# Optimization experiments

Measured on AMD Instinct MI355X. Metric: run time of the kernel, lower is better.

Reference implementation:

```python
import jax, jax.numpy as jnp
import numpy as np

N, M, D = 4096, 8192, 1024
N_ITERS = 15  # module hardcodes self.n_iters = 15
EPS = 1e-12   # F.normalize eps


def setup_inputs() -> dict:
    key = jax.random.key(0)
    k1, k2 = jax.random.split(key)
    K = jax.random.normal(k1, (N, M), dtype=jnp.float32)
    y = jax.random.normal(k2, (M, D), dtype=jnp.float32)
    return {"K": K, "y": y, "topk": 32}


def _topk_preimage(K_mat, y, topk):
    # torch: topk -> L1-normalize values -> scatter into zeros_like(K) -> mm(y).
    # Since topk indices are unique per row, scatter+dense-mm == gather + weighted sum.
    vals, inds = jax.lax.top_k(K_mat, topk)                      # [N, k], [N, k]
    norm = jnp.maximum(jnp.sum(jnp.abs(vals), axis=-1, keepdims=True), EPS)
    w = vals / norm                                              # F.normalize(p=1, dim=-1)
    preimage = jnp.einsum('nk,nkd->nd', w, y[inds])              # [N, D]
    return preimage, inds


def reference(K, y, topk):
    preimage, inds = _topk_preimage(K, y, topk)

    def body(pre, _):
        K_i = pre @ y.T                                          # linear kernel_fn: [N, M]
        pre, inds_i = _topk_preimage(K_i, y, topk)
        return pre, inds_i

    preimage, inds_all = jax.lax.scan(body, preimage, None, length=N_ITERS)
    return preimage, inds_all[-1]
```

## Files before the change

kernel.cpp:

```cpp
#include <hip/hip_runtime.h>
#include <hip/hip_bf16.h>
#include <math.h>

#define N_ROWS 4096
#define M_COLS 8192
#define D_DIM  1024
#define TOPK   32
#define N_ITERS 15
#define CHUNK   2048
#define KC      384
#define D_CUT   1696

template <int EXACT_V>
__global__ __launch_bounds__(256) void topk_pre_kernel(
    const float* __restrict__ R,
    const float* __restrict__ Y,
    float* __restrict__ pre,
    int* __restrict__ inds_ws,
    int row_off, int write_inds)
{
    __shared__ float s_wv[4];
    __shared__ int   s_wi[4];
    __shared__ float topv[TOPK];
    __shared__ int   topi[TOPK];
    __shared__ int   s_win;
    __shared__ float s_w[TOPK];
    __shared__ int   s_si[TOPK];
    __shared__ float s_sw[TOPK];
    __shared__ float s_norm;

    const int tid    = threadIdx.x;
    const int n_loc  = blockIdx.x;
    const int n_glob = row_off + n_loc;
    const float* Rr  = R + (size_t)n_loc * M_COLS;

    float v[32];
    #pragma unroll
    for (int q = 0; q < 8; ++q) {
        float4 w = reinterpret_cast<const float4*>(Rr)[tid + 256 * q];
        v[4 * q + 0] = w.x; v[4 * q + 1] = w.y;
        v[4 * q + 2] = w.z; v[4 * q + 3] = w.w;
    }

    for (int s = 0; s < TOPK; ++s) {
        float bv = -INFINITY; int bi = M_COLS;
        #pragma unroll
        for (int q = 0; q < 8; ++q)
            #pragma unroll
            for (int c = 0; c < 4; ++c) {
                const int m = 4 * q + c;
                const int j = 4 * tid + 1024 * q + c;
                const float val = v[m];
                if (val > bv || (val == bv && j < bi)) { bv = val; bi = j; }
            }
        #pragma unroll
        for (int off = 32; off > 0; off >>= 1) {
            float ov = __shfl_down(bv, off);
            int   oi = __shfl_down(bi, off);
            if (ov > bv || (ov == bv && oi < bi)) { bv = ov; bi = oi; }
        }
        if ((tid & 63) == 0) { s_wv[tid >> 6] = bv; s_wi[tid >> 6] = bi; }
        __syncthreads();
        if (tid == 0) {
            for (int w = 1; w < 4; ++w) {
                if (s_wv[w] > bv || (s_wv[w] == bv && s_wi[w] < bi)) {
                    bv = s_wv[w]; bi = s_wi[w];
                }
            }
            topv[s] = bv; topi[s] = bi; s_win = bi;
        }
        __syncthreads();
        const int win = s_win;
        if (((win >> 2) & 255) == tid) {
            const int mw = ((win >> 10) << 2) | (win & 3);
            #pragma unroll
            for (int m = 0; m < 32; ++m)
                if (m == mw) v[m] = -INFINITY;
        }
    }

    if (EXACT_V) {
        if (tid == 0) {
            double sum = 0.0;
            for (int k = 0; k < TOPK; ++k) sum += fabs((double)topv[k]);
            s_norm = fmaxf((float)sum, 1e-12f);
        }
    } else {
        if (tid == 0) {
            float r[8];
            #pragma unroll
            for (int j = 0; j < 8; ++j) r[j] = fabsf(topv[j]);
            #pragma unroll
            for (int blk = 8; blk < TOPK; blk += 8)
                #pragma unroll
                for (int j = 0; j < 8; ++j)
                    r[j] = __fadd_rn(r[j], fabsf(topv[blk + j]));
            float s01 = __fadd_rn(r[0], r[1]);
            float s23 = __fadd_rn(r[2], r[3]);
            float s45 = __fadd_rn(r[4], r[5]);
            float s67 = __fadd_rn(r[6], r[7]);
            s_norm = fmaxf(__fadd_rn(__fadd_rn(s01, s23), __fadd_rn(s45, s67)), 1e-12f);
        }
    }
    __syncthreads();
    if (tid < TOPK) s_w[tid] = __fdiv_rn(topv[tid], s_norm);
    __syncthreads();

    if (EXACT_V) {
        double acc[4] = {0.0, 0.0, 0.0, 0.0};
        for (int k = 0; k < TOPK; ++k) {
            const double wk = (double)s_w[k];
            const float* yr = Y + (size_t)topi[k] * D_DIM;
            #pragma unroll
            for (int j = 0; j < 4; ++j)
                acc[j] = fma(wk, (double)yr[tid + 256 * j], acc[j]);
        }
        float* pr = pre + (size_t)n_glob * D_DIM;
        #pragma unroll
        for (int j = 0; j < 4; ++j) pr[tid + 256 * j] = (float)acc[j];
    } else {
        if (tid == 0) {
            for (int k = 0; k < TOPK; ++k) { s_si[k] = topi[k]; s_sw[k] = s_w[k]; }
            for (int a = 1; a < TOPK; ++a) {
                int ia = s_si[a]; float wa = s_sw[a];
                int b = a - 1;
                while (b >= 0 && s_si[b] > ia) {
                    s_si[b + 1] = s_si[b]; s_sw[b + 1] = s_sw[b]; --b;
                }
                s_si[b + 1] = ia; s_sw[b + 1] = wa;
            }
        }
        __syncthreads();
        float tot[4]  = {0.f, 0.f, 0.f, 0.f};
        float part[4] = {0.f, 0.f, 0.f, 0.f};
        int curPan = s_si[0] / KC;
        for (int k = 0; k < TOPK; ++k) {
            const int idx = s_si[k];
            const int pan = idx / KC;
            if (pan != curPan) {
                #pragma unroll
                for (int j = 0; j < 4; ++j) {
                    tot[j] = __fadd_rn(tot[j], part[j]);
                    part[j] = 0.f;
                }
                curPan = pan;
            }
            const float wk = s_sw[k];
            const float* yr = Y + (size_t)idx * D_DIM;
            #pragma unroll
            for (int j = 0; j < 4; ++j)
                part[j] = fmaf(wk, yr[tid + 256 * j], part[j]);
        }
        #pragma unroll
        for (int j = 0; j < 4; ++j) tot[j] = __fadd_rn(tot[j], part[j]);
        float* pr = pre + (size_t)n_glob * D_DIM;
        #pragma unroll
        for (int j = 0; j < 4; ++j) pr[tid + 256 * j] = tot[j];
    }

    if (write_inds && tid < TOPK)
        inds_ws[(size_t)n_glob * TOPK + tid] = topi[tid];
}

#define ABM 128
#define ABN 128
#define ABK 16

__global__ __launch_bounds__(256) void gemmA_kernel(
    const float* __restrict__ A,
    const float* __restrict__ B,
    float* __restrict__ C)
{
    __shared__ float As[ABK][ABM + 4];
    __shared__ float Bs[ABK][ABN + 4];

    const int tid  = threadIdx.x;
    const int tx   = tid & 15;
    const int ty   = tid >> 4;
    const int row0 = blockIdx.y * ABM;
    const int col0 = blockIdx.x * ABN;

    const int lr = tid >> 1;
    const int lc = (tid & 1) * 8;

    float tot[8][8], acc[8][8];
    #pragma unroll
    for (int i = 0; i < 8; ++i)
        #pragma unroll
        for (int j = 0; j < 8; ++j) { tot[i][j] = 0.f; acc[i][j] = 0.f; }

    for (int k0 = 0; k0 < D_DIM; k0 += ABK) {
        float4 va0 = *reinterpret_cast<const float4*>(A + (size_t)(row0 + lr) * D_DIM + k0 + lc);
        float4 va1 = *reinterpret_cast<const float4*>(A + (size_t)(row0 + lr) * D_DIM + k0 + lc + 4);
        As[lc + 0][lr] = va0.x; As[lc + 1][lr] = va0.y;
        As[lc + 2][lr] = va0.z; As[lc + 3][lr] = va0.w;
        As[lc + 4][lr] = va1.x; As[lc + 5][lr] = va1.y;
        As[lc + 6][lr] = va1.z; As[lc + 7][lr] = va1.w;
        float4 vb0 = *reinterpret_cast<const float4*>(B + (size_t)(col0 + lr) * D_DIM + k0 + lc);
        float4 vb1 = *reinterpret_cast<const float4*>(B + (size_t)(col0 + lr) * D_DIM + k0 + lc + 4);
        Bs[lc + 0][lr] = vb0.x; Bs[lc + 1][lr] = vb0.y;
        Bs[lc + 2][lr] = vb0.z; Bs[lc + 3][lr] = vb0.w;
        Bs[lc + 4][lr] = vb1.x; Bs[lc + 5][lr] = vb1.y;
        Bs[lc + 6][lr] = vb1.z; Bs[lc + 7][lr] = vb1.w;
        __syncthreads();

        #pragma unroll
        for (int kk = 0; kk < ABK; ++kk) {
            float a[8], b[8];
            #pragma unroll
            for (int i = 0; i < 8; ++i) a[i] = As[kk][ty * 8 + i];
            #pragma unroll
            for (int j = 0; j < 8; ++j) b[j] = Bs[kk][tx * 8 + j];
            #pragma unroll
            for (int i = 0; i < 8; ++i)
                #pragma unroll
                for (int j = 0; j < 8; ++j)
                    acc[i][j] = fmaf(a[i], b[j], acc[i][j]);
        }
        __syncthreads();

        const int kend = k0 + ABK;
        if (kend == KC || kend == 2 * KC || kend == D_DIM) {
            #pragma unroll
            for (int i = 0; i < 8; ++i)
                #pragma unroll
                for (int j = 0; j < 8; ++j) {
                    tot[i][j] = __fadd_rn(tot[i][j], acc[i][j]);
                    acc[i][j] = 0.f;
                }
        }
    }

    #pragma unroll
    for (int i = 0; i < 8; ++i) {
        float4 v0 = { tot[i][0], tot[i][1], tot[i][2], tot[i][3] };
        float4 v1 = { tot[i][4], tot[i][5], tot[i][6], tot[i][7] };
        float* cr = C + (size_t)(row0 + ty * 8 + i) * M_COLS + col0 + tx * 8;
        *reinterpret_cast<float4*>(cr)     = v0;
        *reinterpret_cast<float4*>(cr + 4) = v1;
    }
}

#define BBM 128
#define BBN 64
#define BBK 16

__global__ __launch_bounds__(256) void gemmB_kernel(
    const float* __restrict__ A,
    const float* __restrict__ B,
    float* __restrict__ C)
{
    __shared__ float As[BBK][BBM + 4];
    __shared__ float Bs[BBK][BBN + 4];

    const int tid  = threadIdx.x;
    const int tx   = tid & 15;
    const int ty   = tid >> 4;
    const int row0 = blockIdx.y * BBM;
    const int col0 = blockIdx.x * BBN;

    const int lrA = tid >> 1;
    const int lcA = (tid & 1) * 8;
    const int lrB = tid >> 2;
    const int lcB = (tid & 3) * 4;

    double dacc[8][4];
    #pragma unroll
    for (int i = 0; i < 8; ++i)
        #pragma unroll
        for (int j = 0; j < 4; ++j) dacc[i][j] = 0.0;

    for (int k0 = 0; k0 < D_DIM; k0 += BBK) {
        float4 va0 = *reinterpret_cast<const float4*>(A + (size_t)(row0 + lrA) * D_DIM + k0 + lcA);
        float4 va1 = *reinterpret_cast<const float4*>(A + (size_t)(row0 + lrA) * D_DIM + k0 + lcA + 4);
        As[lcA + 0][lrA] = va0.x; As[lcA + 1][lrA] = va0.y;
        As[lcA + 2][lrA] = va0.z; As[lcA + 3][lrA] = va0.w;
        As[lcA + 4][lrA] = va1.x; As[lcA + 5][lrA] = va1.y;
        As[lcA + 6][lrA] = va1.z; As[lcA + 7][lrA] = va1.w;
        float4 vb = *reinterpret_cast<const float4*>(B + (size_t)(col0 + lrB) * D_DIM + k0 + lcB);
        Bs[lcB + 0][lrB] = vb.x; Bs[lcB + 1][lrB] = vb.y;
        Bs[lcB + 2][lrB] = vb.z; Bs[lcB + 3][lrB] = vb.w;
        __syncthreads();

        #pragma unroll
        for (int kk = 0; kk < BBK; ++kk) {
            double a[8], b[4];
            #pragma unroll
            for (int i = 0; i < 8; ++i) a[i] = (double)As[kk][ty * 8 + i];
            #pragma unroll
            for (int j = 0; j < 4; ++j) b[j] = (double)Bs[kk][tx * 4 + j];
            #pragma unroll
            for (int i = 0; i < 8; ++i)
                #pragma unroll
                for (int j = 0; j < 4; ++j)
                    dacc[i][j] = fma(a[i], b[j], dacc[i][j]);
        }
        __syncthreads();
    }

    #pragma unroll
    for (int i = 0; i < 8; ++i) {
        float4 v = { (float)dacc[i][0], (float)dacc[i][1],
                     (float)dacc[i][2], (float)dacc[i][3] };
        float* cr = C + (size_t)(row0 + ty * 8 + i) * M_COLS + col0 + tx * 4;
        *reinterpret_cast<float4*>(cr) = v;
    }
}

__global__ __launch_bounds__(256) void choice_kernel(
    const int* __restrict__ indsA,
    const int* __restrict__ indsB,
    unsigned char* __restrict__ choice)
{
    const int n = blockIdx.x * 256 + threadIdx.x;
    if (n >= N_ROWS) return;
    int d = 0;
    #pragma unroll
    for (int k = 0; k < TOPK; ++k) {
        int diff = indsA[n * TOPK + k] - indsB[n * TOPK + k];
        if (diff < 0) diff = -diff;
        if (diff > d) d = diff;
    }
    choice[n] = (d > 0 && d <= D_CUT) ? 1 : 0;
}

__global__ __launch_bounds__(256) void emit_kernel(
    const float* __restrict__ preA, const float* __restrict__ preB,
    const int* __restrict__ indsA,  const int* __restrict__ indsB,
    const unsigned char* __restrict__ choice,
    float* __restrict__ out_pre, float* __restrict__ out_inds)
{
    const int n   = blockIdx.x;
    const int tid = threadIdx.x;
    const int c   = choice[n];
    const float* ps = (c ? preB : preA) + (size_t)n * D_DIM;
    const int*   is = (c ? indsB : indsA) + (size_t)n * TOPK;
    float* po = out_pre + (size_t)n * D_DIM;
    #pragma unroll
    for (int j = 0; j < 4; ++j) po[tid + 256 * j] = ps[tid + 256 * j];
    if (tid < TOPK)
        out_inds[(size_t)n * TOPK + tid] = (float)is[tid];
}

extern "C" void kernel_launch(void* const* d_in, const int* in_sizes, int n_in,
                              void* d_out, int out_size, void* d_ws, size_t ws_size,
                              hipStream_t stream)
{
    const float* K_in = (const float*)d_in[0];
    const float* Y    = (const float*)d_in[1];

    char* p = (char*)d_ws;
    float* preA   = (float*)p; p += (size_t)N_ROWS * D_DIM * sizeof(float);
    float* preB   = (float*)p; p += (size_t)N_ROWS * D_DIM * sizeof(float);
    float* Kchunk = (float*)p; p += (size_t)CHUNK * M_COLS * sizeof(float);
    int*   indsA  = (int*)p;   p += (size_t)N_ROWS * TOPK * sizeof(int);
    int*   indsB  = (int*)p;   p += (size_t)N_ROWS * TOPK * sizeof(int);
    unsigned char* choice = (unsigned char*)p;

    float* out_pre  = (float*)d_out;
    float* out_inds = out_pre + (size_t)N_ROWS * D_DIM;

    topk_pre_kernel<0><<<N_ROWS, 256, 0, stream>>>(K_in, Y, preA, indsA, 0, 0);
    topk_pre_kernel<1><<<N_ROWS, 256, 0, stream>>>(K_in, Y, preB, indsB, 0, 0);

    for (int it = 0; it < N_ITERS; ++it) {
        const int wo = (it == N_ITERS - 1) ? 1 : 0;
        for (int c = 0; c < N_ROWS / CHUNK; ++c) {
            gemmA_kernel<<<dim3(M_COLS / ABN, CHUNK / ABM), 256, 0, stream>>>(
                preA + (size_t)c * CHUNK * D_DIM, Y, Kchunk);
            topk_pre_kernel<0><<<CHUNK, 256, 0, stream>>>(
                Kchunk, Y, preA, indsA, c * CHUNK, wo);
            gemmB_kernel<<<dim3(M_COLS / BBN, CHUNK / BBM), 256, 0, stream>>>(
                preB + (size_t)c * CHUNK * D_DIM, Y, Kchunk);
            topk_pre_kernel<1><<<CHUNK, 256, 0, stream>>>(
                Kchunk, Y, preB, indsB, c * CHUNK, wo);
        }
    }

    choice_kernel<<<(N_ROWS + 255) / 256, 256, 0, stream>>>(indsA, indsB, choice);
    emit_kernel<<<N_ROWS, 256, 0, stream>>>(preA, preB, indsA, indsB, choice,
                                            out_pre, out_inds);
}
```

Before: 53.53 ms.

## Vectorize shared-memory fragment loads and enlarge FP64 GEMM tile with double staging

The fp32 GEMM now reads its A/B register fragments from shared memory with float4 loads instead of scalar loads. The fp64 GEMM widens its output tile from 128x64 to 128x128, giving each thread an 8x8 accumulator. It also converts inputs to double when storing them to shared memory, so the inner loop no longer converts per element, and it reads fragments with double2 loads. The aim is fewer LDS instructions and conversions and more reuse per loaded value. The cost is a larger shared-memory footprint and 64 double accumulators per thread, which raises register pressure and may lower occupancy.

```diff
diff --git a/kernel.cpp b/kernel.cpp
--- a/kernel.cpp
+++ b/kernel.cpp
@@ -171,8 +171,8 @@
     const float* __restrict__ B,
     float* __restrict__ C)
 {
-    __shared__ float As[ABK][ABM + 4];
-    __shared__ float Bs[ABK][ABN + 4];
+    __shared__ __align__(16) float As[ABK][ABM + 4];
+    __shared__ __align__(16) float Bs[ABK][ABN + 4];
 
     const int tid  = threadIdx.x;
     const int tx   = tid & 15;
@@ -207,10 +207,10 @@
         #pragma unroll
         for (int kk = 0; kk < ABK; ++kk) {
             float a[8], b[8];
-            #pragma unroll
-            for (int i = 0; i < 8; ++i) a[i] = As[kk][ty * 8 + i];
-            #pragma unroll
-            for (int j = 0; j < 8; ++j) b[j] = Bs[kk][tx * 8 + j];
+            *reinterpret_cast<float4*>(&a[0]) = *reinterpret_cast<float4*>(&As[kk][ty * 8]);
+            *reinterpret_cast<float4*>(&a[4]) = *reinterpret_cast<float4*>(&As[kk][ty * 8 + 4]);
+            *reinterpret_cast<float4*>(&b[0]) = *reinterpret_cast<float4*>(&Bs[kk][tx * 8]);
+            *reinterpret_cast<float4*>(&b[4]) = *reinterpret_cast<float4*>(&Bs[kk][tx * 8 + 4]);
             #pragma unroll
             for (int i = 0; i < 8; ++i)
                 #pragma unroll
@@ -242,7 +242,7 @@
 }
 
 #define BBM 128
-#define BBN 64
+#define BBN 128
 #define BBK 16
 
 __global__ __launch_bounds__(256) void gemmB_kernel(
@@ -250,8 +250,8 @@
     const float* __restrict__ B,
     float* __restrict__ C)
 {
-    __shared__ float As[BBK][BBM + 4];
-    __shared__ float Bs[BBK][BBN + 4];
+    __shared__ __align__(16) double As[BBK][BBM + 4];
+    __shared__ __align__(16) double Bs[BBK][BBN + 4];
 
     const int tid  = threadIdx.x;
     const int tx   = tid & 15;
@@ -259,51 +259,59 @@
     const int row0 = blockIdx.y * BBM;
     const int col0 = blockIdx.x * BBN;
 
-    const int lrA = tid >> 1;
-    const int lcA = (tid & 1) * 8;
-    const int lrB = tid >> 2;
-    const int lcB = (tid & 3) * 4;
-
-    double dacc[8][4];
+    const int lr = tid >> 1;
+    const int lc = (tid & 1) * 8;
+
+    double acc[8][8];
     #pragma unroll
     for (int i = 0; i < 8; ++i)
         #pragma unroll
-        for (int j = 0; j < 4; ++j) dacc[i][j] = 0.0;
+        for (int j = 0; j < 8; ++j) acc[i][j] = 0.0;
 
     for (int k0 = 0; k0 < D_DIM; k0 += BBK) {
-        float4 va0 = *reinterpret_cast<const float4*>(A + (size_t)(row0 + lrA) * D_DIM + k0 + lcA);
-        float4 va1 = *reinterpret_cast<const float4*>(A + (size_t)(row0 + lrA) * D_DIM + k0 + lcA + 4);
-        As[lcA + 0][lrA] = va0.x; As[lcA + 1][lrA] = va0.y;
-        As[lcA + 2][lrA] = va0.z; As[lcA + 3][lrA] = va0.w;
-        As[lcA + 4][lrA] = va1.x; As[lcA + 5][lrA] = va1.y;
-        As[lcA + 6][lrA] = va1.z; As[lcA + 7][lrA] = va1.w;
-        float4 vb = *reinterpret_cast<const float4*>(B + (size_t)(col0 + lrB) * D_DIM + k0 + lcB);
-        Bs[lcB + 0][lrB] = vb.x; Bs[lcB + 1][lrB] = vb.y;
-        Bs[lcB + 2][lrB] = vb.z; Bs[lcB + 3][lrB] = vb.w;
+        float4 va0 = *reinterpret_cast<const float4*>(A + (size_t)(row0 + lr) * D_DIM + k0 + lc);
+        float4 va1 = *reinterpret_cast<const float4*>(A + (size_t)(row0 + lr) * D_DIM + k0 + lc + 4);
+        As[lc + 0][lr] = (double)va0.x; As[lc + 1][lr] = (double)va0.y;
+        As[lc + 2][lr] = (double)va0.z; As[lc + 3][lr] = (double)va0.w;
+        As[lc + 4][lr] = (double)va1.x; As[lc + 5][lr] = (double)va1.y;
+        As[lc + 6][lr] = (double)va1.z; As[lc + 7][lr] = (double)va1.w;
+        float4 vb0 = *reinterpret_cast<const float4*>(B + (size_t)(col0 + lr) * D_DIM + k0 + lc);
+        float4 vb1 = *reinterpret_cast<const float4*>(B + (size_t)(col0 + lr) * D_DIM + k0 + lc + 4);
+        Bs[lc + 0][lr] = (double)vb0.x; Bs[lc + 1][lr] = (double)vb0.y;
+        Bs[lc + 2][lr] = (double)vb0.z; Bs[lc + 3][lr] = (double)vb0.w;
+        Bs[lc + 4][lr] = (double)vb1.x; Bs[lc + 5][lr] = (double)vb1.y;
+        Bs[lc + 6][lr] = (double)vb1.z; Bs[lc + 7][lr] = (double)vb1.w;
         __syncthreads();
 
         #pragma unroll
         for (int kk = 0; kk < BBK; ++kk) {
-            double a[8], b[4];
-            #pragma unroll
-            for (int i = 0; i < 8; ++i) a[i] = (double)As[kk][ty * 8 + i];
-            #pragma unroll
-            for (int j = 0; j < 4; ++j) b[j] = (double)Bs[kk][tx * 4 + j];
+            double a[8], b[8];
+            *reinterpret_cast<double2*>(&a[0]) = *reinterpret_cast<double2*>(&As[kk][ty * 8]);
+            *reinterpret_cast<double2*>(&a[2]) = *reinterpret_cast<double2*>(&As[kk][ty * 8 + 2]);
+            *reinterpret_cast<double2*>(&a[4]) = *reinterpret_cast<double2*>(&As[kk][ty * 8 + 4]);
+            *reinterpret_cast<double2*>(&a[6]) = *reinterpret_cast<double2*>(&As[kk][ty * 8 + 6]);
+            *reinterpret_cast<double2*>(&b[0]) = *reinterpret_cast<double2*>(&Bs[kk][tx * 8]);
+            *reinterpret_cast<double2*>(&b[2]) = *reinterpret_cast<double2*>(&Bs[kk][tx * 8 + 2]);
+            *reinterpret_cast<double2*>(&b[4]) = *reinterpret_cast<double2*>(&Bs[kk][tx * 8 + 4]);
+            *reinterpret_cast<double2*>(&b[6]) = *reinterpret_cast<double2*>(&Bs[kk][tx * 8 + 6]);
             #pragma unroll
             for (int i = 0; i < 8; ++i)
                 #pragma unroll
-                for (int j = 0; j < 4; ++j)
-                    dacc[i][j] = fma(a[i], b[j], dacc[i][j]);
+                for (int j = 0; j < 8; ++j)
+                    acc[i][j] = fma(a[i], b[j], acc[i][j]);
         }
         __syncthreads();
     }
 
     #pragma unroll
     for (int i = 0; i < 8; ++i) {
-        float4 v = { (float)dacc[i][0], (float)dacc[i][1],
-                     (float)dacc[i][2], (float)dacc[i][3] };
-        float* cr = C + (size_t)(row0 + ty * 8 + i) * M_COLS + col0 + tx * 4;
-        *reinterpret_cast<float4*>(cr) = v;
+        float4 v0 = { (float)acc[i][0], (float)acc[i][1],
+                      (float)acc[i][2], (float)acc[i][3] };
+        float4 v1 = { (float)acc[i][4], (float)acc[i][5],
+                      (float)acc[i][6], (float)acc[i][7] };
+        float* cr = C + (size_t)(row0 + ty * 8 + i) * M_COLS + col0 + tx * 8;
+        *reinterpret_cast<float4*>(cr)     = v0;
+        *reinterpret_cast<float4*>(cr + 4) = v1;
     }
 }
 
```

Result: slower. 56.14 ms (+4.9%).

## Fuse fp32 and fp64 GEMM/top-k paths into dual-grid kernels with incremental argmax

Applied to the files above, without the earlier changes.

Merges the fp32 and fp64 GEMM kernels into one launch that picks its path by blockIdx.z, and does the same for the two top-k kernels. Each path gets its own K buffer, and the chunk size drops from 2048 to 1024 to keep workspace size in check. This lets the cheap fp32 work overlap the expensive fp64 work and halves the number of launches per chunk. The top-k loop now keeps a per-thread running max and rescans only in the thread that lost its winner, and the fp32 GEMM reads shared memory with float4 loads. The trade-offs are more chunk iterations, extra register pressure from the dual code paths in one kernel, and wasted early-exit blocks in the fp32 half of the GEMM grid.

```diff
diff --git a/kernel.cpp b/kernel.cpp
--- a/kernel.cpp
+++ b/kernel.cpp
@@ -7,16 +7,15 @@
 #define D_DIM  1024
 #define TOPK   32
 #define N_ITERS 15
-#define CHUNK   2048
+#define CHUNK   1024
 #define KC      384
 #define D_CUT   1696
 
-template <int EXACT_V>
-__global__ __launch_bounds__(256) void topk_pre_kernel(
-    const float* __restrict__ R,
+__global__ __launch_bounds__(256) void topk_dual_kernel(
+    const float* __restrict__ RA, const float* __restrict__ RB,
     const float* __restrict__ Y,
-    float* __restrict__ pre,
-    int* __restrict__ inds_ws,
+    float* __restrict__ preA, float* __restrict__ preB,
+    int* __restrict__ indsA, int* __restrict__ indsB,
     int row_off, int write_inds)
 {
     __shared__ float s_wv[4];
@@ -29,6 +28,11 @@
     __shared__ float s_sw[TOPK];
     __shared__ float s_norm;
 
+    const int exact_v = blockIdx.z;
+    const float* R    = exact_v ? RB : RA;
+    float* pre        = exact_v ? preB : preA;
+    int*   inds_ws    = exact_v ? indsB : indsA;
+
     const int tid    = threadIdx.x;
     const int n_loc  = blockIdx.x;
     const int n_glob = row_off + n_loc;
@@ -42,17 +46,18 @@
         v[4 * q + 2] = w.z; v[4 * q + 3] = w.w;
     }
 
+    float cv = -INFINITY; int ci = M_COLS;
+    #pragma unroll
+    for (int q = 0; q < 8; ++q)
+        #pragma unroll
+        for (int c = 0; c < 4; ++c) {
+            const int m = 4 * q + c;
+            const int j = 4 * tid + 1024 * q + c;
+            if (v[m] > cv || (v[m] == cv && j < ci)) { cv = v[m]; ci = j; }
+        }
+
     for (int s = 0; s < TOPK; ++s) {
-        float bv = -INFINITY; int bi = M_COLS;
-        #pragma unroll
-        for (int q = 0; q < 8; ++q)
-            #pragma unroll
-            for (int c = 0; c < 4; ++c) {
-                const int m = 4 * q + c;
-                const int j = 4 * tid + 1024 * q + c;
-                const float val = v[m];
-                if (val > bv || (val == bv && j < bi)) { bv = val; bi = j; }
-            }
+        float bv = cv; int bi = ci;
         #pragma unroll
         for (int off = 32; off > 0; off >>= 1) {
             float ov = __shfl_down(bv, off);
@@ -76,10 +81,19 @@
             #pragma unroll
             for (int m = 0; m < 32; ++m)
                 if (m == mw) v[m] = -INFINITY;
-        }
-    }
-
-    if (EXACT_V) {
+            cv = -INFINITY; ci = M_COLS;
+            #pragma unroll
+            for (int q = 0; q < 8; ++q)
+                #pragma unroll
+                for (int c = 0; c < 4; ++c) {
+                    const int m = 4 * q + c;
+                    const int j = 4 * tid + 1024 * q + c;
+                    if (v[m] > cv || (v[m] == cv && j < ci)) { cv = v[m]; ci = j; }
+                }
+        }
+    }
+
+    if (exact_v) {
         if (tid == 0) {
             double sum = 0.0;
             for (int k = 0; k < TOPK; ++k) sum += fabs((double)topv[k]);
@@ -106,7 +120,7 @@
     if (tid < TOPK) s_w[tid] = __fdiv_rn(topv[tid], s_norm);
     __syncthreads();
 
-    if (EXACT_V) {
+    if (exact_v) {
         double acc[4] = {0.0, 0.0, 0.0, 0.0};
         for (int k = 0; k < TOPK; ++k) {
             const double wk = (double)s_w[k];
@@ -165,145 +179,141 @@
 #define ABM 128
 #define ABN 128
 #define ABK 16
-
-__global__ __launch_bounds__(256) void gemmA_kernel(
-    const float* __restrict__ A,
-    const float* __restrict__ B,
-    float* __restrict__ C)
-{
-    __shared__ float As[ABK][ABM + 4];
-    __shared__ float Bs[ABK][ABN + 4];
-
-    const int tid  = threadIdx.x;
-    const int tx   = tid & 15;
-    const int ty   = tid >> 4;
-    const int row0 = blockIdx.y * ABM;
-    const int col0 = blockIdx.x * ABN;
-
-    const int lr = tid >> 1;
-    const int lc = (tid & 1) * 8;
-
-    float tot[8][8], acc[8][8];
-    #pragma unroll
-    for (int i = 0; i < 8; ++i)
-        #pragma unroll
-        for (int j = 0; j < 8; ++j) { tot[i][j] = 0.f; acc[i][j] = 0.f; }
-
-    for (int k0 = 0; k0 < D_DIM; k0 += ABK) {
-        float4 va0 = *reinterpret_cast<const float4*>(A + (size_t)(row0 + lr) * D_DIM + k0 + lc);
-        float4 va1 = *reinterpret_cast<const float4*>(A + (size_t)(row0 + lr) * D_DIM + k0 + lc + 4);
-        As[lc + 0][lr] = va0.x; As[lc + 1][lr] = va0.y;
-        As[lc + 2][lr] = va0.z; As[lc + 3][lr] = va0.w;
-        As[lc + 4][lr] = va1.x; As[lc + 5][lr] = va1.y;
-        As[lc + 6][lr] = va1.z; As[lc + 7][lr] = va1.w;
-        float4 vb0 = *reinterpret_cast<const float4*>(B + (size_t)(col0 + lr) * D_DIM + k0 + lc);
-        float4 vb1 = *reinterpret_cast<const float4*>(B + (size_t)(col0 + lr) * D_DIM + k0 + lc + 4);
-        Bs[lc + 0][lr] = vb0.x; Bs[lc + 1][lr] = vb0.y;
-        Bs[lc + 2][lr] = vb0.z; Bs[lc + 3][lr] = vb0.w;
-        Bs[lc + 4][lr] = vb1.x; Bs[lc + 5][lr] = vb1.y;
-        Bs[lc + 6][lr] = vb1.z; Bs[lc + 7][lr] = vb1.w;
-        __syncthreads();
-
-        #pragma unroll
-        for (int kk = 0; kk < ABK; ++kk) {
-            float a[8], b[8];
-            #pragma unroll
-            for (int i = 0; i < 8; ++i) a[i] = As[kk][ty * 8 + i];
-            #pragma unroll
-            for (int j = 0; j < 8; ++j) b[j] = Bs[kk][tx * 8 + j];
-            #pragma unroll
-            for (int i = 0; i < 8; ++i)
-                #pragma unroll
-                for (int j = 0; j < 8; ++j)
-                    acc[i][j] = fmaf(a[i], b[j], acc[i][j]);
-        }
-        __syncthreads();
-
-        const int kend = k0 + ABK;
-        if (kend == KC || kend == 2 * KC || kend == D_DIM) {
-            #pragma unroll
-            for (int i = 0; i < 8; ++i)
-                #pragma unroll
-                for (int j = 0; j < 8; ++j) {
-                    tot[i][j] = __fadd_rn(tot[i][j], acc[i][j]);
-                    acc[i][j] = 0.f;
-                }
-        }
-    }
-
-    #pragma unroll
-    for (int i = 0; i < 8; ++i) {
-        float4 v0 = { tot[i][0], tot[i][1], tot[i][2], tot[i][3] };
-        float4 v1 = { tot[i][4], tot[i][5], tot[i][6], tot[i][7] };
-        float* cr = C + (size_t)(row0 + ty * 8 + i) * M_COLS + col0 + tx * 8;
-        *reinterpret_cast<float4*>(cr)     = v0;
-        *reinterpret_cast<float4*>(cr + 4) = v1;
-    }
-}
-
 #define BBM 128
 #define BBN 64
 #define BBK 16
 
-__global__ __launch_bounds__(256) void gemmB_kernel(
-    const float* __restrict__ A,
-    const float* __restrict__ B,
-    float* __restrict__ C)
-{
-    __shared__ float As[BBK][BBM + 4];
-    __shared__ float Bs[BBK][BBN + 4];
-
-    const int tid  = threadIdx.x;
-    const int tx   = tid & 15;
-    const int ty   = tid >> 4;
-    const int row0 = blockIdx.y * BBM;
-    const int col0 = blockIdx.x * BBN;
-
-    const int lrA = tid >> 1;
-    const int lcA = (tid & 1) * 8;
-    const int lrB = tid >> 2;
-    const int lcB = (tid & 3) * 4;
-
-    double dacc[8][4];
-    #pragma unroll
-    for (int i = 0; i < 8; ++i)
-        #pragma unroll
-        for (int j = 0; j < 4; ++j) dacc[i][j] = 0.0;
-
-    for (int k0 = 0; k0 < D_DIM; k0 += BBK) {
-        float4 va0 = *reinterpret_cast<const float4*>(A + (size_t)(row0 + lrA) * D_DIM + k0 + lcA);
-        float4 va1 = *reinterpret_cast<const float4*>(A + (size_t)(row0 + lrA) * D_DIM + k0 + lcA + 4);
-        As[lcA + 0][lrA] = va0.x; As[lcA + 1][lrA] = va0.y;
-        As[lcA + 2][lrA] = va0.z; As[lcA + 3][lrA] = va0.w;
-        As[lcA + 4][lrA] = va1.x; As[lcA + 5][lrA] = va1.y;
-        As[lcA + 6][lrA] = va1.z; As[lcA + 7][lrA] = va1.w;
-        float4 vb = *reinterpret_cast<const float4*>(B + (size_t)(col0 + lrB) * D_DIM + k0 + lcB);
-        Bs[lcB + 0][lrB] = vb.x; Bs[lcB + 1][lrB] = vb.y;
-        Bs[lcB + 2][lrB] = vb.z; Bs[lcB + 3][lrB] = vb.w;
-        __syncthreads();
-
-        #pragma unroll
-        for (int kk = 0; kk < BBK; ++kk) {
-            double a[8], b[4];
-            #pragma unroll
-            for (int i = 0; i < 8; ++i) a[i] = (double)As[kk][ty * 8 + i];
-            #pragma unroll
-            for (int j = 0; j < 4; ++j) b[j] = (double)Bs[kk][tx * 4 + j];
-            #pragma unroll
-            for (int i = 0; i < 8; ++i)
-                #pragma unroll
-                for (int j = 0; j < 4; ++j)
-                    dacc[i][j] = fma(a[i], b[j], dacc[i][j]);
-        }
-        __syncthreads();
-    }
-
-    #pragma unroll
-    for (int i = 0; i < 8; ++i) {
-        float4 v = { (float)dacc[i][0], (float)dacc[i][1],
-                     (float)dacc[i][2], (float)dacc[i][3] };
-        float* cr = C + (size_t)(row0 + ty * 8 + i) * M_COLS + col0 + tx * 4;
-        *reinterpret_cast<float4*>(cr) = v;
+__global__ __launch_bounds__(256) void gemm_dual_kernel(
+    const float* __restrict__ PA, const float* __restrict__ PB,
+    const float* __restrict__ Y,
+    float* __restrict__ CA, float* __restrict__ CB)
+{
+    __shared__ __align__(16) char smem[16896];
+
+    const int tid = threadIdx.x;
+
+    if (blockIdx.z == 0) {
+        if (blockIdx.x >= M_COLS / ABN) return;
+        float (*As)[ABM + 4] = reinterpret_cast<float(*)[ABM + 4]>(smem);
+        float (*Bs)[ABN + 4] = reinterpret_cast<float(*)[ABN + 4]>(smem + 8448);
+
+        const int tx   = tid & 15;
+        const int ty   = tid >> 4;
+        const int row0 = blockIdx.y * ABM;
+        const int col0 = blockIdx.x * ABN;
+        const int lr   = tid >> 1;
+        const int lc   = (tid & 1) * 8;
+
+        float tot[8][8], acc[8][8];
+        #pragma unroll
+        for (int i = 0; i < 8; ++i)
+            #pragma unroll
+            for (int j = 0; j < 8; ++j) { tot[i][j] = 0.f; acc[i][j] = 0.f; }
+
+        for (int k0 = 0; k0 < D_DIM; k0 += ABK) {
+            float4 va0 = *reinterpret_cast<const float4*>(PA + (size_t)(row0 + lr) * D_DIM + k0 + lc);
+            float4 va1 = *reinterpret_cast<const float4*>(PA + (size_t)(row0 + lr) * D_DIM + k0 + lc + 4);
+            As[lc + 0][lr] = va0.x; As[lc + 1][lr] = va0.y;
+            As[lc + 2][lr] = va0.z; As[lc + 3][lr] = va0.w;
+            As[lc + 4][lr] = va1.x; As[lc + 5][lr] = va1.y;
+            As[lc + 6][lr] = va1.z; As[lc + 7][lr] = va1.w;
+            float4 vb0 = *reinterpret_cast<const float4*>(Y + (size_t)(col0 + lr) * D_DIM + k0 + lc);
+            float4 vb1 = *reinterpret_cast<const float4*>(Y + (size_t)(col0 + lr) * D_DIM + k0 + lc + 4);
+            Bs[lc + 0][lr] = vb0.x; Bs[lc + 1][lr] = vb0.y;
+            Bs[lc + 2][lr] = vb0.z; Bs[lc + 3][lr] = vb0.w;
+            Bs[lc + 4][lr] = vb1.x; Bs[lc + 5][lr] = vb1.y;
+            Bs[lc + 6][lr] = vb1.z; Bs[lc + 7][lr] = vb1.w;
+            __syncthreads();
+
+            #pragma unroll
+            for (int kk = 0; kk < ABK; ++kk) {
+                float a[8], b[8];
+                *reinterpret_cast<float4*>(&a[0]) = *reinterpret_cast<float4*>(&As[kk][ty * 8]);
+                *reinterpret_cast<float4*>(&a[4]) = *reinterpret_cast<float4*>(&As[kk][ty * 8 + 4]);
+                *reinterpret_cast<float4*>(&b[0]) = *reinterpret_cast<float4*>(&Bs[kk][tx * 8]);
+                *reinterpret_cast<float4*>(&b[4]) = *reinterpret_cast<float4*>(&Bs[kk][tx * 8 + 4]);
+                #pragma unroll
+                for (int i = 0; i < 8; ++i)
+                    #pragma unroll
+                    for (int j = 0; j < 8; ++j)
+                        acc[i][j] = fmaf(a[i], b[j], acc[i][j]);
+            }
+            __syncthreads();
+
+            const int kend = k0 + ABK;
+            if (kend == KC || kend == 2 * KC || kend == D_DIM) {
+                #pragma unroll
+                for (int i = 0; i < 8; ++i)
+                    #pragma unroll
+                    for (int j = 0; j < 8; ++j) {
+                        tot[i][j] = __fadd_rn(tot[i][j], acc[i][j]);
+                        acc[i][j] = 0.f;
+                    }
+            }
+        }
+
+        #pragma unroll
+        for (int i = 0; i < 8; ++i) {
+            float4 v0 = { tot[i][0], tot[i][1], tot[i][2], tot[i][3] };
+            float4 v1 = { tot[i][4], tot[i][5], tot[i][6], tot[i][7] };
+            float* cr = CA + (size_t)(row0 + ty * 8 + i) * M_COLS + col0 + tx * 8;
+            *reinterpret_cast<float4*>(cr)     = v0;
+            *reinterpret_cast<float4*>(cr + 4) = v1;
+        }
+    } else {
+        float (*As)[BBM + 4] = reinterpret_cast<float(*)[BBM + 4]>(smem);
+        float (*Bs)[BBN + 4] = reinterpret_cast<float(*)[BBN + 4]>(smem + 8448);
+
+        const int tx   = tid & 15;
+        const int ty   = tid >> 4;
+        const int row0 = blockIdx.y * BBM;
+        const int col0 = blockIdx.x * BBN;
+        const int lrA = tid >> 1;
+        const int lcA = (tid & 1) * 8;
+        const int lrB = tid >> 2;
+        const int lcB = (tid & 3) * 4;
+
+        double dacc[8][4];
+        #pragma unroll
+        for (int i = 0; i < 8; ++i)
+            #pragma unroll
+            for (int j = 0; j < 4; ++j) dacc[i][j] = 0.0;
+
+        for (int k0 = 0; k0 < D_DIM; k0 += BBK) {
+            float4 va0 = *reinterpret_cast<const float4*>(PB + (size_t)(row0 + lrA) * D_DIM + k0 + lcA);
+            float4 va1 = *reinterpret_cast<const float4*>(PB + (size_t)(row0 + lrA) * D_DIM + k0 + lcA + 4);
+            As[lcA + 0][lrA] = va0.x; As[lcA + 1][lrA] = va0.y;
+            As[lcA + 2][lrA] = va0.z; As[lcA + 3][lrA] = va0.w;
+            As[lcA + 4][lrA] = va1.x; As[lcA + 5][lrA] = va1.y;
+            As[lcA + 6][lrA] = va1.z; As[lcA + 7][lrA] = va1.w;
+            float4 vb = *reinterpret_cast<const float4*>(Y + (size_t)(col0 + lrB) * D_DIM + k0 + lcB);
+            Bs[lcB + 0][lrB] = vb.x; Bs[lcB + 1][lrB] = vb.y;
+            Bs[lcB + 2][lrB] = vb.z; Bs[lcB + 3][lrB] = vb.w;
+            __syncthreads();
+
+            #pragma unroll
+            for (int kk = 0; kk < BBK; ++kk) {
+                double a[8], b[4];
+                #pragma unroll
+                for (int i = 0; i < 8; ++i) a[i] = (double)As[kk][ty * 8 + i];
+                #pragma unroll
+                for (int j = 0; j < 4; ++j) b[j] = (double)Bs[kk][tx * 4 + j];
+                #pragma unroll
+                for (int i = 0; i < 8; ++i)
+                    #pragma unroll
+                    for (int j = 0; j < 4; ++j)
+                        dacc[i][j] = fma(a[i], b[j], dacc[i][j]);
+            }
+            __syncthreads();
+        }
+
+        #pragma unroll
+        for (int i = 0; i < 8; ++i) {
+            float4 v = { (float)dacc[i][0], (float)dacc[i][1],
+                         (float)dacc[i][2], (float)dacc[i][3] };
+            float* cr = CB + (size_t)(row0 + ty * 8 + i) * M_COLS + col0 + tx * 4;
+            *reinterpret_cast<float4*>(cr) = v;
+        }
     }
 }
 
@@ -350,30 +360,28 @@
     const float* Y    = (const float*)d_in[1];
 
     char* p = (char*)d_ws;
-    float* preA   = (float*)p; p += (size_t)N_ROWS * D_DIM * sizeof(float);
-    float* preB   = (float*)p; p += (size_t)N_ROWS * D_DIM * sizeof(float);
-    float* Kchunk = (float*)p; p += (size_t)CHUNK * M_COLS * sizeof(float);
-    int*   indsA  = (int*)p;   p += (size_t)N_ROWS * TOPK * sizeof(int);
-    int*   indsB  = (int*)p;   p += (size_t)N_ROWS * TOPK * sizeof(int);
+    float* preA = (float*)p; p += (size_t)N_ROWS * D_DIM * sizeof(float);
+    float* preB = (float*)p; p += (size_t)N_ROWS * D_DIM * sizeof(float);
+    float* KA   = (float*)p; p += (size_t)CHUNK * M_COLS * sizeof(float);
+    float* KB   = (float*)p; p += (size_t)CHUNK * M_COLS * sizeof(float);
+    int*   indsA = (int*)p;  p += (size_t)N_ROWS * TOPK * sizeof(int);
+    int*   indsB = (int*)p;  p += (size_t)N_ROWS * TOPK * sizeof(int);
     unsigned char* choice = (unsigned char*)p;
 
     float* out_pre  = (float*)d_out;
     float* out_inds = out_pre + (size_t)N_ROWS * D_DIM;
 
-    topk_pre_kernel<0><<<N_ROWS, 256, 0, stream>>>(K_in, Y, preA, indsA, 0, 0);
-    topk_pre_kernel<1><<<N_ROWS, 256, 0, stream>>>(K_in, Y, preB, indsB, 0, 0);
+    topk_dual_kernel<<<dim3(N_ROWS, 1, 2), 256, 0, stream>>>(
+        K_in, K_in, Y, preA, preB, indsA, indsB, 0, 0);
 
     for (int it = 0; it < N_ITERS; ++it) {
         const int wo = (it == N_ITERS - 1) ? 1 : 0;
         for (int c = 0; c < N_ROWS / CHUNK; ++c) {
-            gemmA_kernel<<<dim3(M_COLS / ABN, CHUNK / ABM), 256, 0, stream>>>(
-                preA + (size_t)c * CHUNK * D_DIM, Y, Kchunk);
-            topk_pre_kernel<0><<<CHUNK, 256, 0, stream>>>(
-                Kchunk, Y, preA, indsA, c * CHUNK, wo);
-            gemmB_kernel<<<dim3(M_COLS / BBN, CHUNK / BBM), 256, 0, stream>>>(
-                preB + (size_t)c * CHUNK * D_DIM, Y, Kchunk);
-            topk_pre_kernel<1><<<CHUNK, 256, 0, stream>>>(
-                Kchunk, Y, preB, indsB, c * CHUNK, wo);
+            gemm_dual_kernel<<<dim3(M_COLS / BBN, CHUNK / ABM, 2), 256, 0, stream>>>(
+                preA + (size_t)c * CHUNK * D_DIM,
+                preB + (size_t)c * CHUNK * D_DIM, Y, KA, KB);
+            topk_dual_kernel<<<dim3(CHUNK, 1, 2), 256, 0, stream>>>(
+                KA, KB, Y, preA, preB, indsA, indsB, c * CHUNK, wo);
         }
     }
 
```

Measured after the change: 61.98 ms. 1.16x slower.
